# Kernel tuning notes

Measured on AMD Instinct MI355X. Metric: run time of the kernel, lower is better.

The kernel has to match this reference:

```python
import math
import jax, jax.numpy as jnp
import numpy as np

HEAD_DIM = 128
NUM_HEADS = 16
ROPE_BASE = 10000.0


def _rope_tables(seq_len, dim, dtype):
    inv_freq = 1.0 / (ROPE_BASE ** (jnp.arange(0, dim, 2, dtype=jnp.float32) / dim))
    t = jnp.arange(seq_len, dtype=jnp.float32)
    freqs = jnp.einsum('i,j->ij', t, inv_freq)          # [S, D/2]
    emb = jnp.concatenate([freqs, freqs], axis=-1)       # [S, D]
    return jnp.cos(emb).astype(dtype), jnp.sin(emb).astype(dtype)


def _rotate_half(x):
    x1, x2 = jnp.split(x, 2, axis=-1)
    return jnp.concatenate([-x2, x1], axis=-1)


def _apply_rope(x, cos, sin):
    # x: [B, S, H, D]; cos/sin: [S, D] broadcast over batch and heads
    return x * cos[None, :, None, :] + _rotate_half(x) * sin[None, :, None, :]


def setup_inputs() -> dict:
    key = jax.random.key(0)
    k1, k2, k3 = jax.random.split(key, 3)
    B, S, dim = 2, 2048, 2048
    out_dim = (NUM_HEADS + 2 * NUM_HEADS) * HEAD_DIM  # kvph=1 -> 3*H*D = 6144
    x = jax.random.normal(k1, (B, S, dim), dtype=jnp.float32)
    w_qkv = jax.random.normal(k2, (out_dim, dim), dtype=jnp.float32) * 0.02
    w_out = jax.random.normal(k3, (dim, NUM_HEADS * HEAD_DIM), dtype=jnp.float32) * 0.02
    return {"x": x, "w_qkv": w_qkv, "w_out": w_out}


def reference(x, w_qkv, w_out):
    B, S, _ = x.shape
    H, D = NUM_HEADS, HEAD_DIM
    qkv = jnp.einsum('bsd,od->bso', x, w_qkv)            # [B, S, 3*H*D]
    qkv = qkv.reshape(B, S, 3 * H, D)
    q = qkv[:, :, :H, :]                                 # [B, S, H, D]
    k = qkv[:, :, H:2 * H, :]
    v = qkv[:, :, 2 * H:, :]
    cos, sin = _rope_tables(S, D, x.dtype)
    q = _apply_rope(q, cos, sin)
    k = _apply_rope(k, cos, sin)
    scale = 1.0 / math.sqrt(D)
    logits = jnp.einsum('bqhd,bkhd->bhqk', q, k) * scale  # [B, H, S, S]
    attn = jax.nn.softmax(logits.astype(jnp.float32), axis=-1).astype(logits.dtype)
    out = jnp.einsum('bhqk,bkhd->bqhd', attn, v)          # [B, S, H, D]
    out = out.reshape(B, S, H * D)
    return jnp.einsum('bso,do->bsd', out, w_out)
```

## Files before the change

### kernel.cpp

```cpp
#include <hip/hip_runtime.h>
#include <math.h>
#include <stdint.h>

typedef unsigned short u16;
typedef unsigned int u32;
typedef float f32x4 __attribute__((ext_vector_type(4)));
typedef __bf16 bf16x8 __attribute__((ext_vector_type(8)));

typedef const __attribute__((address_space(1))) u32* gas1;
typedef __attribute__((address_space(3))) u32* las3;

#define B_ 2
#define S_ 2048
#define DM_ 2048
#define H_ 16
#define HD_ 128
#define NO_ 6144
#define M_ 4096

__device__ __forceinline__ u16 f2bf(float f) {
  u32 u = __float_as_uint(f);
  u32 r = (u + 0x7fffu + ((u >> 16) & 1u)) >> 16;
  return (u16)r;
}
__device__ __forceinline__ float bf2f(u16 h) {
  return __uint_as_float(((u32)h) << 16);
}

__global__ void cvt_bf16(const float* __restrict__ in, u16* __restrict__ out, int n) {
  int i = (blockIdx.x * blockDim.x + threadIdx.x) * 4;
  int stride = gridDim.x * blockDim.x * 4;
  for (; i < n; i += stride) {
    float4 v = *(const float4*)(in + i);
    ushort4 o;
    o.x = f2bf(v.x); o.y = f2bf(v.y); o.z = f2bf(v.z); o.w = f2bf(v.w);
    *(ushort4*)(out + i) = o;
  }
}

__global__ void rope_tables(float* __restrict__ ct, float* __restrict__ st) {
  int i = blockIdx.x * blockDim.x + threadIdx.x;
  int s = i >> 6, j = i & 63;
  float inv = powf(10000.0f, -(float)j / 64.0f);
  float f = (float)s * inv;
  ct[i] = cosf(f);
  st[i] = sinf(f);
}

__global__ __launch_bounds__(512, 2) void gemm8_bt(const u16* __restrict__ A,
                                                   const u16* __restrict__ B,
                                                   u16* __restrict__ C,
                                                   int M, int N, int K) {
  __shared__ u16 lds8[2][2][2][8192];
  const int t = threadIdx.x;
  const int w = t >> 6, l = t & 63, lr = l & 15, lg = l >> 4;
  const int wm = w >> 2, wn = w & 3;
  const int m0 = blockIdx.y * 256, n0 = blockIdx.x * 256;
  const int r0 = t >> 2;
  const int c = (t & 3) ^ ((t >> 3) & 3);
  const int swr = (lr >> 1) & 3;
  const u16* pA0 = A + (size_t)(m0 + r0) * K + c * 8;
  const u16* pB0 = B + (size_t)(n0 + r0) * K + c * 8;
  const size_t j1 = (size_t)128 * K;

  f32x4 acc[8][4] = {};
  bf16x8 af[8], bq[4];

  const int NT = K / 64, NI = NT / 2;

#define STG(T_, kh_, op_, buf_)                                                      \
  do {                                                                               \
    const u16* s_ = (op_ ? pB0 : pA0) + (T_) * 64 + (kh_) * 32;                      \
    u16* d_ = &lds8[buf_][op_][kh_][0] + w * 512;                                    \
    __builtin_amdgcn_global_load_lds((gas1)s_, (las3)d_, 16, 0, 0);                  \
    __builtin_amdgcn_global_load_lds((gas1)(s_ + j1), (las3)(d_ + 4096), 16, 0, 0);  \
  } while (0)

#define LDF(buf_, kh_)                                                            \
  do {                                                                            \
    const u16* a_ = &lds8[buf_][0][kh_][0];                                       \
    const u16* b_ = &lds8[buf_][1][kh_][0];                                       \
    _Pragma("unroll") for (int mi = 0; mi < 8; ++mi)                              \
        af[mi] = *(const bf16x8*)&a_[(wm * 128 + mi * 16 + lr) * 32 +             \
                                     ((lg ^ swr) * 8)];                           \
    _Pragma("unroll") for (int ni = 0; ni < 4; ++ni)                              \
        bq[ni] = *(const bf16x8*)&b_[(wn * 64 + ni * 16 + lr) * 32 +              \
                                     ((lg ^ swr) * 8)];                           \
  } while (0)

#define MFH(h_)                                                                \
  do {                                                                         \
    __builtin_amdgcn_s_setprio(1);                                             \
    _Pragma("unroll") for (int mi = 0; mi < 4; ++mi)                           \
        _Pragma("unroll") for (int ni = 0; ni < 4; ++ni)                       \
            acc[(h_) * 4 + mi][ni] = __builtin_amdgcn_mfma_f32_16x16x32_bf16(  \
                af[(h_) * 4 + mi], bq[ni], acc[(h_) * 4 + mi][ni], 0, 0, 0);   \
    __builtin_amdgcn_s_setprio(0);                                             \
  } while (0)

#define BAR() __builtin_amdgcn_s_barrier()
#define LGKM0() asm volatile("s_waitcnt lgkmcnt(0)" ::: "memory")
#define VM6() asm volatile("s_waitcnt vmcnt(6)" ::: "memory")

  STG(0, 0, 0, 0); STG(0, 0, 1, 0); STG(0, 1, 0, 0); STG(0, 1, 1, 0);
  STG(1, 0, 0, 1); STG(1, 0, 1, 1); STG(1, 1, 0, 1);
  VM6();
  BAR();

  for (int i = 0; i < NI; ++i) {
    const int T = 2 * i;
    const int Tp2 = (T + 2 < NT) ? T + 2 : NT - 1;
    const int Tp3 = (T + 3 < NT) ? T + 3 : NT - 1;
    LDF(0, 0);
    STG(T + 1, 1, 1, 1);
    BAR(); LGKM0(); MFH(0); BAR();
    STG(Tp2, 0, 0, 0);
    BAR(); MFH(1); BAR();
    LDF(0, 1);
    STG(Tp2, 0, 1, 0);
    BAR(); LGKM0(); MFH(0); BAR();
    STG(Tp2, 1, 0, 0);
    VM6(); BAR(); MFH(1); BAR();
    LDF(1, 0);
    STG(Tp2, 1, 1, 0);
    BAR(); LGKM0(); MFH(0); BAR();
    STG(Tp3, 0, 0, 1);
    BAR(); MFH(1); BAR();
    LDF(1, 1);
    STG(Tp3, 0, 1, 1);
    BAR(); LGKM0(); MFH(0); BAR();
    STG(Tp3, 1, 0, 1);
    VM6(); BAR(); MFH(1); BAR();
  }
  asm volatile("s_waitcnt vmcnt(0)" ::: "memory");
  BAR();

#pragma unroll
  for (int mi = 0; mi < 8; ++mi)
#pragma unroll
    for (int ni = 0; ni < 4; ++ni) {
      int row = m0 + wm * 128 + mi * 16 + lg * 4;
      int col = n0 + wn * 64 + ni * 16 + lr;
#pragma unroll
      for (int j = 0; j < 4; ++j)
        C[(size_t)(row + j) * N + col] = f2bf(acc[mi][ni][j]);
    }
#undef STG
#undef LDF
#undef MFH
#undef BAR
#undef LGKM0
#undef VM6
}

template <int OUT_BF16>
__global__ __launch_bounds__(256) void gemm_bt(const u16* __restrict__ A,
                                               const u16* __restrict__ B,
                                               void* __restrict__ Cv,
                                               int M, int N, int K) {
  __shared__ u16 lA[128 * 32];
  __shared__ u16 lB[128 * 32];
  const int t = threadIdx.x;
  const int m0 = blockIdx.y * 128, n0 = blockIdx.x * 128;
  const int w = t >> 6, l = t & 63, lr = l & 15, lg = l >> 4;
  const int wm = (w >> 1) * 64, wn = (w & 1) * 64;
  f32x4 acc[4][4] = {};
  const int srow = t >> 2;
  const int scol = ((t & 3) ^ ((t >> 3) & 3)) * 8;
  const int swr = (lr >> 1) & 3;
  const u16* Ag = A + (size_t)(m0 + srow) * K + scol;
  const u16* Bg = B + (size_t)(n0 + srow) * K + scol;

  for (int k0 = 0; k0 < K; k0 += 32) {
    __syncthreads();
#pragma unroll
    for (int i = 0; i < 2; i++) {
      __builtin_amdgcn_global_load_lds((gas1)(Ag + (size_t)i * 64 * K + k0),
                                       (las3)(lA + (i * 256 + w * 64) * 8), 16, 0, 0);
      __builtin_amdgcn_global_load_lds((gas1)(Bg + (size_t)i * 64 * K + k0),
                                       (las3)(lB + (i * 256 + w * 64) * 8), 16, 0, 0);
    }
    __syncthreads();
    bf16x8 af[4], bfr[4];
#pragma unroll
    for (int mi = 0; mi < 4; mi++)
      af[mi] = *(const bf16x8*)&lA[(wm + mi * 16 + lr) * 32 + (lg ^ swr) * 8];
#pragma unroll
    for (int ni = 0; ni < 4; ni++)
      bfr[ni] = *(const bf16x8*)&lB[(wn + ni * 16 + lr) * 32 + (lg ^ swr) * 8];
#pragma unroll
    for (int mi = 0; mi < 4; mi++)
#pragma unroll
      for (int ni = 0; ni < 4; ni++)
        acc[mi][ni] =
            __builtin_amdgcn_mfma_f32_16x16x32_bf16(af[mi], bfr[ni], acc[mi][ni], 0, 0, 0);
  }

#pragma unroll
  for (int mi = 0; mi < 4; mi++)
#pragma unroll
    for (int ni = 0; ni < 4; ni++) {
      int row = m0 + wm + mi * 16 + lg * 4;
      int col = n0 + wn + ni * 16 + lr;
      if (OUT_BF16) {
        u16* C = (u16*)Cv;
#pragma unroll
        for (int j = 0; j < 4; j++) C[(size_t)(row + j) * N + col] = f2bf(acc[mi][ni][j]);
      } else {
        float* C = (float*)Cv;
#pragma unroll
        for (int j = 0; j < 4; j++) C[(size_t)(row + j) * N + col] = acc[mi][ni][j];
      }
    }
}

__global__ void rope_apply(u16* __restrict__ qkv, const float* __restrict__ ct,
                           const float* __restrict__ st) {
  int i = blockIdx.x * blockDim.x + threadIdx.x;
  int j = i & 63;
  int hh = (i >> 6) & 31;
  int row = i >> 11;
  int s = row & (S_ - 1);
  int col = (hh < 16) ? hh * 128 : 2048 + (hh - 16) * 128;
  u16* p = qkv + (size_t)row * NO_ + col + j;
  float e1 = bf2f(p[0]), e2 = bf2f(p[64]);
  float c = ct[(s << 6) + j], sn = st[(s << 6) + j];
  float o1 = e1 * c - e2 * sn;
  float o2 = e2 * c + e1 * sn;
  if (hh < 16) {
    const float kq = 0.08838834764831845f * 1.4426950408889634f;
    o1 *= kq;
    o2 *= kq;
  }
  p[0] = f2bf(o1);
  p[64] = f2bf(o2);
}

__global__ __launch_bounds__(256) void transpose_v(const u16* __restrict__ qkv,
                                                   u16* __restrict__ vt) {
  __shared__ u16 lds[128 * 64];
  const int bh = blockIdx.y;
  const int b = bh >> 4, h = bh & 15;
  const int s0 = blockIdx.x * 64;
  const int t = threadIdx.x;
  union { uint4 v; u16 e[8]; } uu;
#pragma unroll
  for (int i = 0; i < 4; i++) {
    int s = i * 16 + (t >> 4);
    int dc = (t & 15) * 8;
    uu.v = *(const uint4*)(qkv + (size_t)(b * S_ + s0 + s) * NO_ + 4096 + h * 128 + dc);
#pragma unroll
    for (int q = 0; q < 8; q++) {
      int d = dc + q;
      lds[d * 64 + (s ^ (((d >> 3) & 7) << 3))] = uu.e[q];
    }
  }
  __syncthreads();
#pragma unroll
  for (int i = 0; i < 4; i++) {
    int d = i * 32 + (t >> 3);
    int sc = (t & 7) * 8;
    uint4 v = *(const uint4*)&lds[d * 64 + (sc ^ (((d >> 3) & 7) << 3))];
    *(uint4*)(vt + (size_t)(bh * 128 + d) * S_ + s0 + sc) = v;
  }
}

__global__ __launch_bounds__(256, 2) void flash_attn(const u16* __restrict__ qkv,
                                                     const u16* __restrict__ vt,
                                                     u16* __restrict__ ao) {
  __shared__ u16 lK[2][64 * 128];
  __shared__ u16 lV[2][128 * 64];
  __shared__ u16 lP[4][2][16 * 64];
  const int t = threadIdx.x;
  const int w = t >> 6, l = t & 63, lr = l & 15, lg = l >> 4;
  const int bh = blockIdx.y, b = bh >> 4, h = bh & 15;
  const int q0 = blockIdx.x * 128;

  bf16x8 qf[2][4];
#pragma unroll
  for (int g = 0; g < 2; g++) {
    const u16* Qg = qkv + (size_t)(b * S_ + q0 + w * 32 + g * 16 + lr) * NO_ + h * 128;
#pragma unroll
    for (int c = 0; c < 4; c++) qf[g][c] = *(const bf16x8*)(Qg + c * 32 + lg * 8);
  }

  f32x4 acc[2][8] = {};
  float m_run[2] = {-INFINITY, -INFINITY};
  float l_run[2] = {0.f, 0.f};

  const u16* ksrc[4];
  const u16* vsrc[4];
#pragma unroll
  for (int q = 0; q < 4; q++) {
    int rt = w * 16 + q * 4 + (l >> 4);
    int ck = (l & 15) ^ (rt & 15);
    ksrc[q] = qkv + (size_t)(b * S_ + rt) * NO_ + 2048 + h * 128 + ck * 8;
    int d = w * 32 + q * 8 + (l >> 3);
    int cv = (l & 7) ^ (d & 7);
    vsrc[q] = vt + (size_t)(bh * 128 + d) * S_ + cv * 8;
  }

#pragma unroll
  for (int q = 0; q < 4; q++) {
    __builtin_amdgcn_global_load_lds((gas1)ksrc[q],
                                     (las3)(lK[0] + (w * 16 + q * 4) * 128), 16, 0, 0);
    __builtin_amdgcn_global_load_lds((gas1)vsrc[q],
                                     (las3)(lV[0] + (w * 32 + q * 8) * 64), 16, 0, 0);
    ksrc[q] += (size_t)64 * NO_;
    vsrc[q] += 64;
  }
  __syncthreads();

  const int NT = S_ / 64;
  for (int kt = 0; kt < NT; kt++) {
    const int cur = kt & 1;
    if (kt + 1 < NT) {
#pragma unroll
      for (int q = 0; q < 4; q++) {
        __builtin_amdgcn_global_load_lds((gas1)ksrc[q],
                                         (las3)(lK[cur ^ 1] + (w * 16 + q * 4) * 128), 16, 0, 0);
        __builtin_amdgcn_global_load_lds((gas1)vsrc[q],
                                         (las3)(lV[cur ^ 1] + (w * 32 + q * 8) * 64), 16, 0, 0);
        ksrc[q] += (size_t)64 * NO_;
        vsrc[q] += 64;
      }
    }

    f32x4 sc[2][4];
#pragma unroll
    for (int g = 0; g < 2; g++)
#pragma unroll
      for (int cb = 0; cb < 4; cb++) sc[g][cb] = (f32x4){0.f, 0.f, 0.f, 0.f};
    __builtin_amdgcn_s_setprio(1);
#pragma unroll
    for (int cb = 0; cb < 4; cb++) {
      int r = cb * 16 + lr;
#pragma unroll
      for (int c = 0; c < 4; c++) {
        bf16x8 kf = *(const bf16x8*)&lK[cur][r * 128 + ((c * 32 + lg * 8) ^ ((r & 15) << 3))];
        sc[0][cb] = __builtin_amdgcn_mfma_f32_16x16x32_bf16(kf, qf[0][c], sc[0][cb], 0, 0, 0);
        sc[1][cb] = __builtin_amdgcn_mfma_f32_16x16x32_bf16(kf, qf[1][c], sc[1][cb], 0, 0, 0);
      }
    }
    __builtin_amdgcn_s_setprio(0);

    float tmax[2];
#pragma unroll
    for (int g = 0; g < 2; g++) {
      float v = sc[g][0][0];
#pragma unroll
      for (int cb = 0; cb < 4; cb++)
#pragma unroll
        for (int j = 0; j < 4; j++) v = fmaxf(v, sc[g][cb][j]);
      v = fmaxf(v, __shfl_xor(v, 16));
      v = fmaxf(v, __shfl_xor(v, 32));
      tmax[g] = v;
    }
    bool ok = (tmax[0] <= m_run[0] + 10.0f) && (tmax[1] <= m_run[1] + 10.0f);
    if (!__all(ok)) {
      float resc[2];
#pragma unroll
      for (int g = 0; g < 2; g++) {
        float mn = fmaxf(m_run[g], tmax[g]);
        resc[g] = exp2f(m_run[g] - mn);
        m_run[g] = mn;
        l_run[g] *= resc[g];
      }
#pragma unroll
      for (int g = 0; g < 2; g++)
#pragma unroll
        for (int j = 0; j < 4; j++) {
          float rj = __shfl(resc[g], lg * 4 + j);
#pragma unroll
          for (int nb = 0; nb < 8; nb++) acc[g][nb][j] *= rj;
        }
    }
#pragma unroll
    for (int g = 0; g < 2; g++) {
      float ps = 0.f;
#pragma unroll
      for (int cb = 0; cb < 4; cb++)
#pragma unroll
        for (int j = 0; j < 4; j++) {
          float p = exp2f(sc[g][cb][j] - m_run[g]);
          sc[g][cb][j] = p;
          ps += p;
        }
      ps += __shfl_xor(ps, 16);
      ps += __shfl_xor(ps, 32);
      l_run[g] += ps;
    }

#pragma unroll
    for (int g = 0; g < 2; g++) {
      u16* lPw = lP[w][g];
#pragma unroll
      for (int cb = 0; cb < 4; cb++) {
        ushort4 pk;
        pk.x = f2bf(sc[g][cb][0]);
        pk.y = f2bf(sc[g][cb][1]);
        pk.z = f2bf(sc[g][cb][2]);
        pk.w = f2bf(sc[g][cb][3]);
        *(ushort4*)&lPw[lr * 64 + ((cb * 16 + lg * 4) ^ ((lr & 7) << 3))] = pk;
      }
    }

    __builtin_amdgcn_s_setprio(1);
#pragma unroll
    for (int c2 = 0; c2 < 2; c2++) {
      bf16x8 pf0 = *(const bf16x8*)&lP[w][0][lr * 64 + ((c2 * 32 + lg * 8) ^ ((lr & 7) << 3))];
      bf16x8 pf1 = *(const bf16x8*)&lP[w][1][lr * 64 + ((c2 * 32 + lg * 8) ^ ((lr & 7) << 3))];
#pragma unroll
      for (int nb = 0; nb < 8; nb++) {
        int r = nb * 16 + lr;
        bf16x8 vf = *(const bf16x8*)&lV[cur][r * 64 + ((c2 * 32 + lg * 8) ^ ((r & 7) << 3))];
        acc[0][nb] = __builtin_amdgcn_mfma_f32_16x16x32_bf16(pf0, vf, acc[0][nb], 0, 0, 0);
        acc[1][nb] = __builtin_amdgcn_mfma_f32_16x16x32_bf16(pf1, vf, acc[1][nb], 0, 0, 0);
      }
    }
    __builtin_amdgcn_s_setprio(0);

    __syncthreads();
  }

#pragma unroll
  for (int g = 0; g < 2; g++) {
    float linv[4];
#pragma unroll
    for (int j = 0; j < 4; j++) linv[j] = 1.0f / __shfl(l_run[g], lg * 4 + j);
#pragma unroll
    for (int nb = 0; nb < 8; nb++)
#pragma unroll
      for (int j = 0; j < 4; j++) {
        int qrow = q0 + w * 32 + g * 16 + lg * 4 + j;
        ao[(size_t)(b * S_ + qrow) * 2048 + h * 128 + nb * 16 + lr] =
            f2bf(acc[g][nb][j] * linv[j]);
      }
  }
}

extern "C" void kernel_launch(void* const* d_in, const int* in_sizes, int n_in,
                              void* d_out, int out_size, void* d_ws, size_t ws_size,
                              hipStream_t stream) {
  const float* x = (const float*)d_in[0];
  const float* wqkv = (const float*)d_in[1];
  const float* wout = (const float*)d_in[2];
  float* out = (float*)d_out;

  char* ws = (char*)d_ws;
  u16* xbf = (u16*)(ws);
  u16* wqkvb = (u16*)(ws + ((size_t)16 << 20));
  u16* woutb = (u16*)(ws + ((size_t)40 << 20));
  u16* qkv = (u16*)(ws + ((size_t)48 << 20));
  u16* vtb = (u16*)(ws + ((size_t)96 << 20));
  float* ct = (float*)(ws + ((size_t)112 << 20));
  float* st = (float*)(ws + ((size_t)112 << 20) + ((size_t)1 << 19));
  u16* aout = xbf;

  cvt_bf16<<<4096, 256, 0, stream>>>(x, xbf, M_ * DM_);
  cvt_bf16<<<4096, 256, 0, stream>>>(wqkv, wqkvb, NO_ * DM_);
  cvt_bf16<<<4096, 256, 0, stream>>>(wout, woutb, DM_ * DM_);
  rope_tables<<<(S_ * 64) / 256, 256, 0, stream>>>(ct, st);
  gemm8_bt<<<dim3(NO_ / 256, M_ / 256), 512, 0, stream>>>(xbf, wqkvb, qkv, M_, NO_, DM_);
  rope_apply<<<(M_ * 32 * 64) / 256, 256, 0, stream>>>(qkv, ct, st);
  transpose_v<<<dim3(S_ / 64, B_ * H_), 256, 0, stream>>>(qkv, vtb);
  flash_attn<<<dim3(S_ / 128, B_ * H_), 256, 0, stream>>>(qkv, vtb, aout);
  gemm_bt<0><<<dim3(DM_ / 128, M_ / 128), 256, 0, stream>>>(aout, woutb, out, M_, DM_, DM_);
}
```

Measured before the change: 332.9 us.

## Split QKV GEMM for wave quantization, vectorize RoPE, trim softmax shuffles

The QKV projection is split into a 256-tile launch for Q/K and a 128-tile launch for V, writing into the shared buffer via a new ldc argument. The intent is to reduce tail-wave imbalance across CUs. RoPE now processes two adjacent elements per thread with 32-bit and float2 loads. In attention, the per-tile cross-lane row-sum reduction is deferred to the epilogue, and P is packed to bf16 with the hardware packed-convert instruction. The extra launch and the smaller-tile GEMM for V may cost some efficiency.

After: 327.1 us. About the same (-1.7%).

```diff
diff --git a/kernel.cpp b/kernel.cpp
--- a/kernel.cpp
+++ b/kernel.cpp
@@ -50,7 +50,7 @@
 __global__ __launch_bounds__(512, 2) void gemm8_bt(const u16* __restrict__ A,
                                                    const u16* __restrict__ B,
                                                    u16* __restrict__ C,
-                                                   int M, int N, int K) {
+                                                   int M, int N, int K, int ldc) {
   __shared__ u16 lds8[2][2][2][8192];
   const int t = threadIdx.x;
   const int w = t >> 6, l = t & 63, lr = l & 15, lg = l >> 4;
@@ -143,7 +143,7 @@
       int col = n0 + wn * 64 + ni * 16 + lr;
 #pragma unroll
       for (int j = 0; j < 4; ++j)
-        C[(size_t)(row + j) * N + col] = f2bf(acc[mi][ni][j]);
+        C[(size_t)(row + j) * ldc + col] = f2bf(acc[mi][ni][j]);
     }
 #undef STG
 #undef LDF
@@ -157,7 +157,7 @@
 __global__ __launch_bounds__(256) void gemm_bt(const u16* __restrict__ A,
                                                const u16* __restrict__ B,
                                                void* __restrict__ Cv,
-                                               int M, int N, int K) {
+                                               int M, int N, int K, int ldc) {
   __shared__ u16 lA[128 * 32];
   __shared__ u16 lB[128 * 32];
   const int t = threadIdx.x;
@@ -205,11 +205,11 @@
       if (OUT_BF16) {
         u16* C = (u16*)Cv;
 #pragma unroll
-        for (int j = 0; j < 4; j++) C[(size_t)(row + j) * N + col] = f2bf(acc[mi][ni][j]);
+        for (int j = 0; j < 4; j++) C[(size_t)(row + j) * ldc + col] = f2bf(acc[mi][ni][j]);
       } else {
         float* C = (float*)Cv;
 #pragma unroll
-        for (int j = 0; j < 4; j++) C[(size_t)(row + j) * N + col] = acc[mi][ni][j];
+        for (int j = 0; j < 4; j++) C[(size_t)(row + j) * ldc + col] = acc[mi][ni][j];
       }
     }
 }
@@ -217,23 +217,28 @@
 __global__ void rope_apply(u16* __restrict__ qkv, const float* __restrict__ ct,
                            const float* __restrict__ st) {
   int i = blockIdx.x * blockDim.x + threadIdx.x;
-  int j = i & 63;
-  int hh = (i >> 6) & 31;
-  int row = i >> 11;
+  int j = (i & 31) * 2;
+  int hh = (i >> 5) & 31;
+  int row = i >> 10;
   int s = row & (S_ - 1);
   int col = (hh < 16) ? hh * 128 : 2048 + (hh - 16) * 128;
   u16* p = qkv + (size_t)row * NO_ + col + j;
-  float e1 = bf2f(p[0]), e2 = bf2f(p[64]);
-  float c = ct[(s << 6) + j], sn = st[(s << 6) + j];
-  float o1 = e1 * c - e2 * sn;
-  float o2 = e2 * c + e1 * sn;
+  u32 a = *(const u32*)&p[0];
+  u32 bm = *(const u32*)&p[64];
+  float2 cc = *(const float2*)&ct[(s << 6) + j];
+  float2 ss = *(const float2*)&st[(s << 6) + j];
+  float e10 = bf2f((u16)a), e11 = bf2f((u16)(a >> 16));
+  float e20 = bf2f((u16)bm), e21 = bf2f((u16)(bm >> 16));
+  float o10 = e10 * cc.x - e20 * ss.x;
+  float o11 = e11 * cc.y - e21 * ss.y;
+  float o20 = e20 * cc.x + e10 * ss.x;
+  float o21 = e21 * cc.y + e11 * ss.y;
   if (hh < 16) {
     const float kq = 0.08838834764831845f * 1.4426950408889634f;
-    o1 *= kq;
-    o2 *= kq;
-  }
-  p[0] = f2bf(o1);
-  p[64] = f2bf(o2);
+    o10 *= kq; o11 *= kq; o20 *= kq; o21 *= kq;
+  }
+  *(u32*)&p[0] = (u32)f2bf(o10) | ((u32)f2bf(o11) << 16);
+  *(u32*)&p[64] = (u32)f2bf(o20) | ((u32)f2bf(o21) << 16);
 }
 
 __global__ __launch_bounds__(256) void transpose_v(const u16* __restrict__ qkv,
@@ -347,11 +352,14 @@
     float tmax[2];
 #pragma unroll
     for (int g = 0; g < 2; g++) {
-      float v = sc[g][0][0];
-#pragma unroll
-      for (int cb = 0; cb < 4; cb++)
-#pragma unroll
-        for (int j = 0; j < 4; j++) v = fmaxf(v, sc[g][cb][j]);
+      float v = fmaxf(fmaxf(sc[g][0][0], sc[g][0][1]), sc[g][0][2]);
+      v = fmaxf(fmaxf(v, sc[g][0][3]), sc[g][1][0]);
+      v = fmaxf(fmaxf(v, sc[g][1][1]), sc[g][1][2]);
+      v = fmaxf(fmaxf(v, sc[g][1][3]), sc[g][2][0]);
+      v = fmaxf(fmaxf(v, sc[g][2][1]), sc[g][2][2]);
+      v = fmaxf(fmaxf(v, sc[g][2][3]), sc[g][3][0]);
+      v = fmaxf(fmaxf(v, sc[g][3][1]), sc[g][3][2]);
+      v = fmaxf(v, sc[g][3][3]);
       v = fmaxf(v, __shfl_xor(v, 16));
       v = fmaxf(v, __shfl_xor(v, 32));
       tmax[g] = v;
@@ -386,8 +394,6 @@
           sc[g][cb][j] = p;
           ps += p;
         }
-      ps += __shfl_xor(ps, 16);
-      ps += __shfl_xor(ps, 32);
       l_run[g] += ps;
     }
 
@@ -396,12 +402,13 @@
       u16* lPw = lP[w][g];
 #pragma unroll
       for (int cb = 0; cb < 4; cb++) {
-        ushort4 pk;
-        pk.x = f2bf(sc[g][cb][0]);
-        pk.y = f2bf(sc[g][cb][1]);
-        pk.z = f2bf(sc[g][cb][2]);
-        pk.w = f2bf(sc[g][cb][3]);
-        *(ushort4*)&lPw[lr * 64 + ((cb * 16 + lg * 4) ^ ((lr & 7) << 3))] = pk;
+        u32 p01, p23;
+        asm("v_cvt_pk_bf16_f32 %0, %1, %2" : "=v"(p01) : "v"(sc[g][cb][0]), "v"(sc[g][cb][1]));
+        asm("v_cvt_pk_bf16_f32 %0, %1, %2" : "=v"(p23) : "v"(sc[g][cb][2]), "v"(sc[g][cb][3]));
+        uint2 pk;
+        pk.x = p01;
+        pk.y = p23;
+        *(uint2*)&lPw[lr * 64 + ((cb * 16 + lg * 4) ^ ((lr & 7) << 3))] = pk;
       }
     }
 
@@ -425,9 +432,12 @@
 
 #pragma unroll
   for (int g = 0; g < 2; g++) {
+    float lsum = l_run[g];
+    lsum += __shfl_xor(lsum, 16);
+    lsum += __shfl_xor(lsum, 32);
     float linv[4];
 #pragma unroll
-    for (int j = 0; j < 4; j++) linv[j] = 1.0f / __shfl(l_run[g], lg * 4 + j);
+    for (int j = 0; j < 4; j++) linv[j] = 1.0f / __shfl(lsum, lg * 4 + j);
 #pragma unroll
     for (int nb = 0; nb < 8; nb++)
 #pragma unroll
@@ -461,9 +471,12 @@
   cvt_bf16<<<4096, 256, 0, stream>>>(wqkv, wqkvb, NO_ * DM_);
   cvt_bf16<<<4096, 256, 0, stream>>>(wout, woutb, DM_ * DM_);
   rope_tables<<<(S_ * 64) / 256, 256, 0, stream>>>(ct, st);
-  gemm8_bt<<<dim3(NO_ / 256, M_ / 256), 512, 0, stream>>>(xbf, wqkvb, qkv, M_, NO_, DM_);
-  rope_apply<<<(M_ * 32 * 64) / 256, 256, 0, stream>>>(qkv, ct, st);
+  gemm8_bt<<<dim3(16, 16), 512, 0, stream>>>(xbf, wqkvb, qkv, M_, 4096, DM_, NO_);
+  gemm_bt<1><<<dim3(16, 32), 256, 0, stream>>>(
+      xbf, wqkvb + (size_t)4096 * DM_, qkv + 4096, M_, 2048, DM_, NO_);
+  rope_apply<<<(M_ * 32 * 32) / 256, 256, 0, stream>>>(qkv, ct, st);
   transpose_v<<<dim3(S_ / 64, B_ * H_), 256, 0, stream>>>(qkv, vtb);
   flash_attn<<<dim3(S_ / 128, B_ * H_), 256, 0, stream>>>(qkv, vtb, aout);
-  gemm_bt<0><<<dim3(DM_ / 128, M_ / 128), 256, 0, stream>>>(aout, woutb, out, M_, DM_, DM_);
-}
+  gemm_bt<0><<<dim3(DM_ / 128, M_ / 128), 256, 0, stream>>>(aout, woutb, out, M_, DM_, DM_,
+                                                            DM_);
+}
```
